# Performance work log

Measured on AMD Instinct MI355X. Metric: run time of the kernel, lower is better.

The kernel has to match this reference:

```python
import jax, jax.numpy as jnp
import numpy as np
from jax import lax

B, DIM, H, W = 4, 256, 128, 128
KS, LOC, STRIDES_CFG, HEADS = 5, [2, 3], [1, 2], 8
C2 = DIM // 2
GK = HEADS * KS  # per-pixel dynamic kernel channels

def _kernel_map(ks, kstride, kloc):
    # replicates LSAMixer.generate_kernel_map_1d
    axes, strides, start = [0], [1], 1
    for loc, s in zip(kloc, kstride):
        for num in range(0, loc - start):
            axes.append(num * s + axes[-1] + strides[-1])
            strides.append(s)
        start = loc
    patch = (axes[-1] + strides[-1]) * 2 - 1
    full_axes = [-a for a in axes[:0:-1]] + axes
    full_strides = strides[:0:-1] + strides
    return full_axes, full_strides, patch

OFFS, STRDS, PATCH = _kernel_map(KS, STRIDES_CFG, LOC)
PAD = PATCH // 2

def _pw(x, w, b):
    # 1x1 conv as GEMM
    return jnp.einsum('bchw,oc->bohw', x, w) + b[None, :, None, None]

def _dw(x, w, b, ph, pw):
    # depthwise conv, torch OIHW layout with I=1
    y = lax.conv_general_dilated(x, w, (1, 1), [(ph, ph), (pw, pw)],
                                 feature_group_count=x.shape[1],
                                 dimension_numbers=('NCHW', 'OIHW', 'NCHW'))
    return y + b[None, :, None, None]

def _fsa(x, kern, groups, axis):
    # dynamic local attention: for each tap k (offset a, stride s) gather the
    # average of x over the s-wide strided window along `axis`, weight it by
    # the per-head dynamic kernel, and accumulate.
    Bx, Cx, Hx, Wx = x.shape
    gd = Cx // groups
    K = len(OFFS)
    L = x.shape[axis]
    padcfg = [(0, 0)] * 4
    padcfg[axis] = (PAD, PAD)
    xp = jnp.pad(x, padcfg)
    taps = []
    for a, s in zip(OFFS, STRDS):
        start = a if a >= 0 else a - s + 1  # window covers s pixels away from center
        acc = lax.slice_in_dim(xp, PAD + start, PAD + start + L, axis=axis)
        for d in range(1, s):
            acc = acc + lax.slice_in_dim(xp, PAD + start + d, PAD + start + d + L, axis=axis)
        taps.append(acc / s)
    t = jnp.stack(taps, 0).reshape(K, Bx, groups, gd, Hx, Wx)
    k = kern.reshape(Bx, groups, K, Hx, Wx)
    return jnp.einsum('kbgdhw,bgkhw->bgdhw', t, k).reshape(Bx, Cx, Hx, Wx)

def setup_inputs() -> dict:
    key = jax.random.key(0)
    ks = jax.random.split(key, 12)
    sc = 0.02
    f32 = jnp.float32
    return {
        'x': jax.random.normal(ks[0], (B, DIM, H, W), f32),
        'proj_in_w': jax.random.normal(ks[1], (DIM, DIM), f32) * sc,
        'proj_in_b': jnp.zeros((DIM,), f32),
        'hk_dw_w': jax.random.normal(ks[2], (C2, 1, 1, PATCH), f32) * sc,
        'hk_dw_b': jnp.zeros((C2,), f32),
        'hk_pw_w': jax.random.normal(ks[3], (GK, C2), f32) * sc,
        'hk_pw_b': jnp.zeros((GK,), f32),
        'vk_dw_w': jax.random.normal(ks[4], (C2, 1, PATCH, 1), f32) * sc,
        'vk_dw_b': jnp.zeros((C2,), f32),
        'vk_pw_w': jax.random.normal(ks[5], (GK, C2), f32) * sc,
        'vk_pw_b': jnp.zeros((GK,), f32),
        'cb_w1': jax.random.normal(ks[6], (DIM // 4, C2), f32) * sc,
        'cb_b1': jnp.zeros((DIM // 4,), f32),
        'cb_w2': jax.random.normal(ks[7], (C2, DIM // 4), f32) * sc,
        'cb_b2': jnp.zeros((C2,), f32),
        'proj_out_w': jax.random.normal(ks[8], (DIM, DIM), f32) * sc,
        'proj_out_b': jnp.zeros((DIM,), f32),
    }

def reference(x, proj_in_w, proj_in_b, hk_dw_w, hk_dw_b, hk_pw_w, hk_pw_b,
              vk_dw_w, vk_dw_b, vk_pw_w, vk_pw_b, cb_w1, cb_b1, cb_w2, cb_b2,
              proj_out_w, proj_out_b):
    Bv, _, Hv, Wv = x.shape
    h = _pw(x, proj_in_w, proj_in_b)
    x1, x2 = h[:, :C2], h[:, C2:]
    # channel branch: pw -> relu -> pw
    x_conv = _pw(jax.nn.relu(_pw(x1, cb_w1, cb_b1)), cb_w2, cb_b2)
    # horizontal dynamic kernel + fsa
    kh = jnp.tanh(_pw(_dw(x2, hk_dw_w, hk_dw_b, 0, PAD), hk_pw_w, hk_pw_b))
    attn_h = _fsa(x2, kh, HEADS, axis=3)
    # vertical dynamic kernel + fsa
    kv = jnp.tanh(_pw(_dw(attn_h, vk_dw_w, vk_dw_b, PAD, 0), vk_pw_w, vk_pw_b))
    attn = _fsa(attn_h, kv, HEADS, axis=2)
    N = Hv * Wv
    xc = x_conv.reshape(Bv, C2, N)
    at = attn.reshape(Bv, C2, N)
    # SpatialInteraction(x_conv, attn): modulates x_conv
    s_sig = jax.nn.sigmoid(jnp.einsum('bc,bcn->bn', at.mean(-1), xc) / C2)[:, None, :]
    spatial_map = (s_sig * xc).reshape(Bv, C2, Hv, Wv)
    # ChannelInteraction(x_conv, attn): modulates attn
    c_sig = jax.nn.sigmoid(jnp.einsum('bcn,bn->bc', at, xc.mean(1)) / N)[:, :, None]
    channel_map = (c_sig * at).reshape(Bv, C2, Hv, Wv)
    out = jnp.concatenate([spatial_map, channel_map], axis=1)
    return _pw(out, proj_out_w, proj_out_b)
```

## Files before the change

### kernel.cpp

```cpp
#include <hip/hip_runtime.h>
#include <hip/hip_bf16.h>
#include <math.h>

typedef __hip_bfloat16 bf16;
typedef __attribute__((ext_vector_type(8))) short short8;
typedef __attribute__((ext_vector_type(4))) float floatx4;
#define DEV __device__ __forceinline__

constexpr int BATCH = 4;
constexpr int DIM   = 256;
constexpr int C2    = 128;
constexpr int GK    = 40;
constexpr int HH    = 128;
constexpr int WW    = 128;
constexpr int NPIX  = HH * WW;
constexpr int TPB   = 256;

DEV float toF(float v) { return v; }
DEV float toF(bf16 v)  { return __bfloat162float(v); }

DEV unsigned short f2bs(float f) {
  union { bf16 h; unsigned short u; } cv;
  cv.h = __float2bfloat16(f);
  return cv.u;
}
DEV float bs2f(unsigned short u) {
  union { float f; unsigned x; } c;
  c.x = ((unsigned)u) << 16;
  return c.f;
}

template<int N>
DEV void load_f32v(const float* __restrict__ p, float* v) {
  if constexpr (N == 8) {
    const float4 a = *(const float4*)p;
    const float4 b = *(const float4*)(p + 4);
    v[0]=a.x; v[1]=a.y; v[2]=a.z; v[3]=a.w; v[4]=b.x; v[5]=b.y; v[6]=b.z; v[7]=b.w;
  } else if constexpr (N == 4) {
    const float4 a = *(const float4*)p;
    v[0]=a.x; v[1]=a.y; v[2]=a.z; v[3]=a.w;
  } else {
    const float2 a = *(const float2*)p;
    v[0]=a.x; v[1]=a.y;
  }
}
template<int N>
DEV void load_bf16v(const bf16* __restrict__ p, float* v) {
  if constexpr (N == 8) {
    const uint4 u = *(const uint4*)p;
    v[0]=bs2f(u.x & 0xffff); v[1]=bs2f(u.x >> 16);
    v[2]=bs2f(u.y & 0xffff); v[3]=bs2f(u.y >> 16);
    v[4]=bs2f(u.z & 0xffff); v[5]=bs2f(u.z >> 16);
    v[6]=bs2f(u.w & 0xffff); v[7]=bs2f(u.w >> 16);
  } else if constexpr (N == 4) {
    const uint2 u = *(const uint2*)p;
    v[0]=bs2f(u.x & 0xffff); v[1]=bs2f(u.x >> 16);
    v[2]=bs2f(u.y & 0xffff); v[3]=bs2f(u.y >> 16);
  } else {
    const unsigned u = *(const unsigned*)p;
    v[0]=bs2f(u & 0xffff); v[1]=bs2f(u >> 16);
  }
}
DEV void load8bf(const bf16* __restrict__ p, float* v) { load_bf16v<8>(p, v); }

__global__ __launch_bounds__(TPB) void prepack_kernel(
    const float* __restrict__ w0, const float* __restrict__ w1,
    const float* __restrict__ w2, const float* __restrict__ w3,
    const float* __restrict__ w4, const float* __restrict__ w5,
    short* __restrict__ dst) {
  const int i = blockIdx.x * TPB + threadIdx.x;
  if (i >= 157696) return;
  int j = i;
  float v;
  if (j < 65536) v = w0[j];
  else if ((j -= 65536) < 8192) v = w1[j];
  else if ((j -= 8192) < 8192) v = w2[j];
  else if ((j -= 8192) < 5120) v = w3[j];
  else if ((j -= 5120) < 5120) v = w4[j];
  else { j -= 5120; v = w5[j]; }
  dst[i] = (short)f2bs(v);
}

template<int K, int O, int ACT, int GATED, int DW, typename TIN, typename TOUT>
__global__ __launch_bounds__(TPB) void pw2_kernel(
    const TIN* __restrict__ in, int in_bs,
    const short* __restrict__ wbf, const float* __restrict__ bias,
    TOUT* __restrict__ out, int out_bs,
    const bf16* __restrict__ gxc, const bf16* __restrict__ gattn,
    const float* __restrict__ gs, const float* __restrict__ gc,
    const float* __restrict__ dww, const float* __restrict__ dwb) {
  constexpr int C8   = K / 8;
  constexpr int PXT  = K / 32;
  constexpr int PG   = 64 / PXT;
  constexpr int ROWB = K * 2 + 16;
  constexpr int WO   = (O + 63) / 64;
  static_assert(DW == 0 || PXT == 4, "DW fusion assumes K=128 staging shape");
  __shared__ char smem[64 * ROWB];

  const int p0   = blockIdx.x * 64;
  const int b    = blockIdx.y;
  const int t    = threadIdx.x;
  const int lane = t & 63, wid = t >> 6;
  const int q    = lane >> 4, i16 = lane & 15;

  {
    const int c8  = t / PG;
    const int px0 = (t % PG) * PXT;
    float vals[8][PXT];
    if constexpr (DW == 1) {
      const int p = p0 + px0;
      const int row = p >> 7, w0 = p & (WW - 1);
#pragma unroll
      for (int j = 0; j < 8; ++j) {
        const int c = c8 * 8 + j;
        const float* xr = (const float*)in + ((size_t)b * C2 + c) * NPIX + row * WW;
        float xs[10];
        if (w0 > 0) { const float4 L = *(const float4*)(xr + w0 - 4); xs[0]=L.y; xs[1]=L.z; xs[2]=L.w; }
        else { xs[0]=xs[1]=xs[2]=0.f; }
        { const float4 A = *(const float4*)(xr + w0); xs[3]=A.x; xs[4]=A.y; xs[5]=A.z; xs[6]=A.w; }
        if (w0 < WW - 4) { const float4 R = *(const float4*)(xr + w0 + 4); xs[7]=R.x; xs[8]=R.y; xs[9]=R.z; }
        else { xs[7]=xs[8]=xs[9]=0.f; }
        float wv[7];
#pragma unroll
        for (int k = 0; k < 7; ++k) wv[k] = dww[c * 7 + k];
        const float bv = dwb[c];
#pragma unroll
        for (int px = 0; px < PXT; ++px) {
          float a = bv;
#pragma unroll
          for (int k = 0; k < 7; ++k) a = fmaf(wv[k], xs[px + k], a);
          vals[j][px] = a;
        }
      }
    } else if constexpr (DW == 2) {
      const int p = p0 + px0;
      const int row = p >> 7, w0 = p & (WW - 1);
#pragma unroll
      for (int j = 0; j < 8; ++j) {
        const int c = c8 * 8 + j;
        const bf16* base = (const bf16*)in + ((size_t)b * C2 + c) * NPIX + w0;
        float rr[7][PXT];
#pragma unroll
        for (int k = 0; k < 7; ++k) {
          const int hq = row - 3 + k;
          if (hq >= 0 && hq < HH) load_bf16v<PXT>(base + (size_t)hq * WW, rr[k]);
          else
#pragma unroll
            for (int px = 0; px < PXT; ++px) rr[k][px] = 0.f;
        }
        float wv[7];
#pragma unroll
        for (int k = 0; k < 7; ++k) wv[k] = dww[c * 7 + k];
        const float bv = dwb[c];
#pragma unroll
        for (int px = 0; px < PXT; ++px) {
          float a = bv;
#pragma unroll
          for (int k = 0; k < 7; ++k) a = fmaf(wv[k], rr[k][px], a);
          vals[j][px] = a;
        }
      }
    } else {
      float svals[PXT];
      if constexpr (GATED) {
        if (c8 < C8 / 2) load_f32v<PXT>(gs + (size_t)b * NPIX + p0 + px0, svals);
      }
#pragma unroll
      for (int j = 0; j < 8; ++j) {
        const int c = c8 * 8 + j;
        float tmp[PXT];
        if constexpr (GATED) {
          if (c < C2) {
            load_bf16v<PXT>(gxc + ((size_t)b * C2 + c) * NPIX + p0 + px0, tmp);
#pragma unroll
            for (int px = 0; px < PXT; ++px) vals[j][px] = tmp[px] * svals[px];
          } else {
            const float cg = gc[b * C2 + (c - C2)];
            load_bf16v<PXT>(gattn + ((size_t)b * C2 + (c - C2)) * NPIX + p0 + px0, tmp);
#pragma unroll
            for (int px = 0; px < PXT; ++px) vals[j][px] = tmp[px] * cg;
          }
        } else {
          const TIN* src = in + ((size_t)b * in_bs + c) * NPIX + p0 + px0;
          if constexpr (sizeof(TIN) == 4) load_f32v<PXT>((const float*)src, tmp);
          else                            load_bf16v<PXT>((const bf16*)src, tmp);
#pragma unroll
          for (int px = 0; px < PXT; ++px) vals[j][px] = tmp[px];
        }
      }
    }
#pragma unroll
    for (int px = 0; px < PXT; ++px) {
      const int p = px0 + px;
      short8 pk;
#pragma unroll
      for (int j = 0; j < 8; ++j) pk[j] = (short)f2bs(vals[j][px]);
      const int phys = c8 ^ ((p >> 3) & 7);
      *reinterpret_cast<short8*>(smem + (size_t)p * ROWB + phys * 16) = pk;
    }
  }
  __syncthreads();

  const int o_base = wid * WO * 16;
  if (o_base >= O) return;

  floatx4 acc[WO][4];
#pragma unroll
  for (int ot = 0; ot < WO; ++ot)
#pragma unroll
    for (int nt = 0; nt < 4; ++nt)
      acc[ot][nt] = (floatx4){0.f, 0.f, 0.f, 0.f};

  for (int kc = 0; kc < K / 32; ++kc) {
    short8 afrag[WO];
#pragma unroll
    for (int ot = 0; ot < WO; ++ot) {
      int o = o_base + ot * 16 + i16;
      if (o >= O) o = O - 1;
      afrag[ot] = *reinterpret_cast<const short8*>(wbf + (size_t)o * K + kc * 32 + q * 8);
    }
    short8 bfrag[4];
#pragma unroll
    for (int nt = 0; nt < 4; ++nt) {
      const int n = nt * 16 + i16;
      const int phys = (kc * 4 + q) ^ ((n >> 3) & 7);
      bfrag[nt] = *reinterpret_cast<const short8*>(smem + (size_t)n * ROWB + phys * 16);
    }
#pragma unroll
    for (int ot = 0; ot < WO; ++ot)
#pragma unroll
      for (int nt = 0; nt < 4; ++nt)
        acc[ot][nt] = __builtin_amdgcn_mfma_f32_16x16x32_bf16(
            afrag[ot], bfrag[nt], acc[ot][nt], 0, 0, 0);
  }

#pragma unroll
  for (int ot = 0; ot < WO; ++ot) {
#pragma unroll
    for (int reg = 0; reg < 4; ++reg) {
      const int o = o_base + ot * 16 + q * 4 + reg;
      if (o < O) {
        const float bv = bias[o];
#pragma unroll
        for (int nt = 0; nt < 4; ++nt) {
          float v = acc[ot][nt][reg] + bv;
          if (ACT == 1) v = fmaxf(v, 0.0f);
          if (ACT == 2) v = tanhf(v);
          TOUT* dst = out + ((size_t)b * out_bs + o) * NPIX + p0 + nt * 16 + i16;
          if constexpr (sizeof(TOUT) == 4) *dst = v;
          else *dst = __float2bfloat16(v);
        }
      }
    }
  }
}

__global__ __launch_bounds__(TPB) void pwfused_kernel(
    const float* __restrict__ x,
    const short* __restrict__ w_pi, const float* __restrict__ pib,
    const short* __restrict__ w_cb1, const float* __restrict__ cbb1,
    const short* __restrict__ w_cb2, const float* __restrict__ cbb2,
    float* __restrict__ x2out, bf16* __restrict__ xconv) {
  constexpr int ROWB  = 256 * 2 + 16;
  constexpr int HROWB = 128 * 2 + 16;
  constexpr int TROWB = 64 * 2 + 16;
  __shared__ char smem[64 * ROWB];
  __shared__ char hbuf[64 * HROWB];
  __shared__ char tbuf[64 * TROWB];

  const int p0   = blockIdx.x * 64;
  const int b    = blockIdx.y;
  const int t    = threadIdx.x;
  const int lane = t & 63, wid = t >> 6;
  const int q    = lane >> 4, i16 = lane & 15;

  {
    const int c8  = t / 8;
    const int px0 = (t % 8) * 8;
    float vals[8][8];
#pragma unroll
    for (int j = 0; j < 8; ++j) {
      const int c = c8 * 8 + j;
      load_f32v<8>(x + ((size_t)b * DIM + c) * NPIX + p0 + px0, vals[j]);
    }
#pragma unroll
    for (int px = 0; px < 8; ++px) {
      const int p = px0 + px;
      short8 pk;
#pragma unroll
      for (int j = 0; j < 8; ++j) pk[j] = (short)f2bs(vals[j][px]);
      const int phys = c8 ^ ((p >> 3) & 7);
      *reinterpret_cast<short8*>(smem + (size_t)p * ROWB + phys * 16) = pk;
    }
  }
  __syncthreads();

  const int o_base = wid * 64;
  {
    floatx4 acc[4][4];
#pragma unroll
    for (int ot = 0; ot < 4; ++ot)
#pragma unroll
      for (int nt = 0; nt < 4; ++nt)
        acc[ot][nt] = (floatx4){0.f, 0.f, 0.f, 0.f};

    for (int kc = 0; kc < 8; ++kc) {
      short8 afrag[4];
#pragma unroll
      for (int ot = 0; ot < 4; ++ot) {
        const int o = o_base + ot * 16 + i16;
        afrag[ot] = *reinterpret_cast<const short8*>(w_pi + (size_t)o * 256 + kc * 32 + q * 8);
      }
      short8 bfrag[4];
#pragma unroll
      for (int nt = 0; nt < 4; ++nt) {
        const int n = nt * 16 + i16;
        const int phys = (kc * 4 + q) ^ ((n >> 3) & 7);
        bfrag[nt] = *reinterpret_cast<const short8*>(smem + (size_t)n * ROWB + phys * 16);
      }
#pragma unroll
      for (int ot = 0; ot < 4; ++ot)
#pragma unroll
        for (int nt = 0; nt < 4; ++nt)
          acc[ot][nt] = __builtin_amdgcn_mfma_f32_16x16x32_bf16(
              afrag[ot], bfrag[nt], acc[ot][nt], 0, 0, 0);
    }

#pragma unroll
    for (int ot = 0; ot < 4; ++ot) {
      const int ch0 = o_base + ot * 16 + q * 4;
      if (ch0 >= C2) {
#pragma unroll
        for (int reg = 0; reg < 4; ++reg) {
          const int o = ch0 + reg;
          const float bv = pib[o];
#pragma unroll
          for (int nt = 0; nt < 4; ++nt)
            x2out[((size_t)b * C2 + (o - C2)) * NPIX + p0 + nt * 16 + i16] =
                acc[ot][nt][reg] + bv;
        }
      } else {
        float bv4[4];
#pragma unroll
        for (int reg = 0; reg < 4; ++reg) bv4[reg] = pib[ch0 + reg];
#pragma unroll
        for (int nt = 0; nt < 4; ++nt) {
          const int px = nt * 16 + i16;
          ushort4 pk;
          pk.x = f2bs(acc[ot][nt][0] + bv4[0]);
          pk.y = f2bs(acc[ot][nt][1] + bv4[1]);
          pk.z = f2bs(acc[ot][nt][2] + bv4[2]);
          pk.w = f2bs(acc[ot][nt][3] + bv4[3]);
          const int phys = (ch0 >> 3) ^ ((px >> 3) & 7);
          *reinterpret_cast<ushort4*>(hbuf + (size_t)px * HROWB + phys * 16 +
                                      (ch0 & 7) * 2) = pk;
        }
      }
    }
  }
  __syncthreads();

  {
    floatx4 acc2[4];
#pragma unroll
    for (int nt = 0; nt < 4; ++nt) acc2[nt] = (floatx4){0.f, 0.f, 0.f, 0.f};
    const int o2b = wid * 16;
    for (int kc = 0; kc < 4; ++kc) {
      const short8 afrag = *reinterpret_cast<const short8*>(
          w_cb1 + (size_t)(o2b + i16) * 128 + kc * 32 + q * 8);
      short8 bfrag[4];
#pragma unroll
      for (int nt = 0; nt < 4; ++nt) {
        const int n = nt * 16 + i16;
        const int phys = (kc * 4 + q) ^ ((n >> 3) & 7);
        bfrag[nt] = *reinterpret_cast<const short8*>(hbuf + (size_t)n * HROWB + phys * 16);
      }
#pragma unroll
      for (int nt = 0; nt < 4; ++nt)
        acc2[nt] = __builtin_amdgcn_mfma_f32_16x16x32_bf16(afrag, bfrag[nt], acc2[nt], 0, 0, 0);
    }
    const int ch0 = o2b + q * 4;
    float bv4[4];
#pragma unroll
    for (int reg = 0; reg < 4; ++reg) bv4[reg] = cbb1[ch0 + reg];
#pragma unroll
    for (int nt = 0; nt < 4; ++nt) {
      const int px = nt * 16 + i16;
      ushort4 pk;
      pk.x = f2bs(fmaxf(acc2[nt][0] + bv4[0], 0.f));
      pk.y = f2bs(fmaxf(acc2[nt][1] + bv4[1], 0.f));
      pk.z = f2bs(fmaxf(acc2[nt][2] + bv4[2], 0.f));
      pk.w = f2bs(fmaxf(acc2[nt][3] + bv4[3], 0.f));
      const int phys = (ch0 >> 3) ^ ((px >> 3) & 7);
      *reinterpret_cast<ushort4*>(tbuf + (size_t)px * TROWB + phys * 16 +
                                  (ch0 & 7) * 2) = pk;
    }
  }
  __syncthreads();

  {
    floatx4 acc3[2][4];
#pragma unroll
    for (int ot = 0; ot < 2; ++ot)
#pragma unroll
      for (int nt = 0; nt < 4; ++nt) acc3[ot][nt] = (floatx4){0.f, 0.f, 0.f, 0.f};
    const int o3b = wid * 32;
    for (int kc = 0; kc < 2; ++kc) {
      short8 afrag[2];
#pragma unroll
      for (int ot = 0; ot < 2; ++ot)
        afrag[ot] = *reinterpret_cast<const short8*>(
            w_cb2 + (size_t)(o3b + ot * 16 + i16) * 64 + kc * 32 + q * 8);
      short8 bfrag[4];
#pragma unroll
      for (int nt = 0; nt < 4; ++nt) {
        const int n = nt * 16 + i16;
        const int phys = (kc * 4 + q) ^ ((n >> 3) & 7);
        bfrag[nt] = *reinterpret_cast<const short8*>(tbuf + (size_t)n * TROWB + phys * 16);
      }
#pragma unroll
      for (int ot = 0; ot < 2; ++ot)
#pragma unroll
        for (int nt = 0; nt < 4; ++nt)
          acc3[ot][nt] = __builtin_amdgcn_mfma_f32_16x16x32_bf16(
              afrag[ot], bfrag[nt], acc3[ot][nt], 0, 0, 0);
    }
#pragma unroll
    for (int ot = 0; ot < 2; ++ot) {
#pragma unroll
      for (int reg = 0; reg < 4; ++reg) {
        const int o = o3b + ot * 16 + q * 4 + reg;
        const float bv = cbb2[o];
#pragma unroll
        for (int nt = 0; nt < 4; ++nt)
          xconv[((size_t)b * C2 + o) * NPIX + p0 + nt * 16 + i16] =
              __float2bfloat16(acc3[ot][nt][reg] + bv);
      }
    }
  }
}

DEV float block_reduce_sum(float v) {
#pragma unroll
  for (int off = 32; off > 0; off >>= 1) v += __shfl_down(v, off, 64);
  __shared__ float ls[TPB / 64];
  const int lane = threadIdx.x & 63;
  const int wid  = threadIdx.x >> 6;
  if (lane == 0) ls[wid] = v;
  __syncthreads();
  float s = 0.0f;
  if (threadIdx.x == 0) {
#pragma unroll
    for (int i = 0; i < TPB / 64; ++i) s += ls[i];
  }
  return s;
}

__global__ __launch_bounds__(TPB) void fsah2_kernel(
    const float* __restrict__ x, int x_bs,
    const bf16* __restrict__ kern, bf16* __restrict__ out) {
  const int g  = blockIdx.x * TPB + threadIdx.x;
  const int w8 = g & 15;
  const int hp = (g >> 4) & (HH - 1);
  const int c  = (g >> 11) & (C2 - 1);
  const int b  = g >> 18;
  const float* xr = x + ((size_t)b * x_bs + c) * NPIX + hp * WW;
  const int px0 = w8 * 8;
  float xs[14];
  if (w8 > 0) { const float4 L = *(const float4*)(xr + px0 - 4); xs[0]=L.y; xs[1]=L.z; xs[2]=L.w; }
  else { xs[0]=xs[1]=xs[2]=0.f; }
  { const float4 a = *(const float4*)(xr + px0);
    const float4 bq = *(const float4*)(xr + px0 + 4);
    xs[3]=a.x; xs[4]=a.y; xs[5]=a.z; xs[6]=a.w;
    xs[7]=bq.x; xs[8]=bq.y; xs[9]=bq.z; xs[10]=bq.w; }
  if (w8 < 15) { const float4 R = *(const float4*)(xr + px0 + 8); xs[11]=R.x; xs[12]=R.y; xs[13]=R.z; }
  else { xs[11]=xs[12]=xs[13]=0.f; }
  float k[5][8];
  const bf16* kr = kern + ((size_t)b * GK + (c >> 4) * 5) * NPIX + hp * WW + px0;
#pragma unroll
  for (int tp = 0; tp < 5; ++tp) load8bf(kr + (size_t)tp * NPIX, k[tp]);
  short8 o;
#pragma unroll
  for (int i = 0; i < 8; ++i) {
    float a = 0.5f * (xs[i] + xs[i + 1]) * k[0][i];
    a = fmaf(xs[i + 2], k[1][i], a);
    a = fmaf(xs[i + 3], k[2][i], a);
    a = fmaf(xs[i + 4], k[3][i], a);
    a = fmaf(0.5f * (xs[i + 5] + xs[i + 6]), k[4][i], a);
    o[i] = (short)f2bs(a);
  }
  *reinterpret_cast<short8*>(out + ((size_t)(b * C2 + c)) * NPIX + hp * WW + px0) = o;
}

__global__ __launch_bounds__(TPB) void fsav2_kernel(
    const bf16* __restrict__ x,
    const bf16* __restrict__ kern, bf16* __restrict__ out,
    float* __restrict__ at_mean) {
  const int g  = blockIdx.x * TPB + threadIdx.x;
  const int w8 = g & 15;
  const int hp = (g >> 4) & (HH - 1);
  const int c  = (g >> 11) & (C2 - 1);
  const int b  = g >> 18;
  const int px0 = w8 * 8;
  const bf16* base = x + ((size_t)(b * C2 + c)) * NPIX + px0;
  float r[7][8];
#pragma unroll
  for (int j = 0; j < 7; ++j) {
    const int hq = hp - 3 + j;
    if (hq >= 0 && hq < HH) load8bf(base + (size_t)hq * WW, r[j]);
    else
#pragma unroll
      for (int i = 0; i < 8; ++i) r[j][i] = 0.f;
  }
  float k[5][8];
  const bf16* kr = kern + ((size_t)b * GK + (c >> 4) * 5) * NPIX + hp * WW + px0;
#pragma unroll
  for (int tp = 0; tp < 5; ++tp) load8bf(kr + (size_t)tp * NPIX, k[tp]);
  short8 o;
  float ps = 0.0f;
#pragma unroll
  for (int i = 0; i < 8; ++i) {
    float a = 0.5f * (r[0][i] + r[1][i]) * k[0][i];
    a = fmaf(r[2][i], k[1][i], a);
    a = fmaf(r[3][i], k[2][i], a);
    a = fmaf(r[4][i], k[3][i], a);
    a = fmaf(0.5f * (r[5][i] + r[6][i]), k[4][i], a);
    o[i] = (short)f2bs(a);
    ps += bs2f((unsigned short)o[i]);
  }
  *reinterpret_cast<short8*>(out + ((size_t)(b * C2 + c)) * NPIX + hp * WW + px0) = o;
  const float s = block_reduce_sum(ps);
  if (threadIdx.x == 0) atomicAdd(&at_mean[b * C2 + c], s);
}

__global__ __launch_bounds__(TPB) void xs_kernel(const bf16* __restrict__ xc,
                                                 const float* __restrict__ at_mean,
                                                 float* __restrict__ xc_mean,
                                                 float* __restrict__ s_sig) {
  __shared__ float am[C2];
  const int b = blockIdx.y;
  if (threadIdx.x < C2) am[threadIdx.x] = at_mean[b * C2 + threadIdx.x] * (1.0f / NPIX);
  __syncthreads();
  const int p = blockIdx.x * TPB + threadIdx.x;
  const bf16* r = xc + (size_t)b * C2 * NPIX + p;
  float s = 0.0f, m = 0.0f;
#pragma unroll 4
  for (int c = 0; c < C2; ++c) {
    const float v = toF(r[(size_t)c * NPIX]);
    m += v;
    s = fmaf(am[c], v, s);
  }
  xc_mean[(size_t)b * NPIX + p] = m * (1.0f / C2);
  s_sig[(size_t)b * NPIX + p]   = 1.0f / (1.0f + expf(-s * (1.0f / C2)));
}

__global__ __launch_bounds__(TPB) void csig_kernel(const bf16* __restrict__ attn,
                                                   const float* __restrict__ xc_mean,
                                                   float* __restrict__ out) {
  const int bc = blockIdx.x;
  const int b  = bc / C2;
  const bf16* r = attn + (size_t)bc * NPIX;
  const float* m = xc_mean + (size_t)b * NPIX;
  float s = 0.0f;
  for (int i = threadIdx.x * 8; i < NPIX; i += TPB * 8) {
    float v[8], mm[8];
    load8bf(r + i, v);
    load_f32v<8>(m + i, mm);
#pragma unroll
    for (int j = 0; j < 8; ++j) s = fmaf(v[j], mm[j], s);
  }
  s = block_reduce_sum(s);
  if (threadIdx.x == 0) out[bc] = 1.0f / (1.0f + expf(-s * (1.0f / NPIX)));
}

extern "C" void kernel_launch(void* const* d_in, const int* in_sizes, int n_in,
                              void* d_out, int out_size, void* d_ws, size_t ws_size,
                              hipStream_t stream) {
  const float* x    = (const float*)d_in[0];
  const float* piw  = (const float*)d_in[1];
  const float* pib  = (const float*)d_in[2];
  const float* hkdw = (const float*)d_in[3];
  const float* hkdb = (const float*)d_in[4];
  const float* hkpw = (const float*)d_in[5];
  const float* hkpb = (const float*)d_in[6];
  const float* vkdw = (const float*)d_in[7];
  const float* vkdb = (const float*)d_in[8];
  const float* vkpw = (const float*)d_in[9];
  const float* vkpb = (const float*)d_in[10];
  const float* cbw1 = (const float*)d_in[11];
  const float* cbb1 = (const float*)d_in[12];
  const float* cbw2 = (const float*)d_in[13];
  const float* cbb2 = (const float*)d_in[14];
  const float* pow_ = (const float*)d_in[15];
  const float* pob  = (const float*)d_in[16];
  float* out = (float*)d_out;

  char* ws = (char*)d_ws;
  size_t off = 0;
  auto alloc = [&](size_t bytes) -> char* {
    char* p = ws + off;
    off += (bytes + 255) & ~(size_t)255;
    return p;
  };
  short* wpk    = (short*)alloc(157696 * 2);
  float* x2buf  = (float*)alloc((size_t)BATCH * C2  * NPIX * 4);
  bf16*  x_conv = (bf16*) alloc((size_t)BATCH * C2  * NPIX * 2);
  bf16*  kbuf   = (bf16*) alloc((size_t)BATCH * GK  * NPIX * 2);
  bf16*  attn_h = (bf16*) alloc((size_t)BATCH * C2  * NPIX * 2);
  bf16*  attn   = (bf16*) alloc((size_t)BATCH * C2  * NPIX * 2);
  float* at_mean = (float*)alloc((size_t)BATCH * C2 * 4);
  float* xc_mean = (float*)alloc((size_t)BATCH * NPIX * 4);
  float* s_sig   = (float*)alloc((size_t)BATCH * NPIX * 4);
  float* c_sig   = (float*)alloc((size_t)BATCH * C2 * 4);

  const short* w_pi  = wpk;
  const short* w_cb1 = wpk + 65536;
  const short* w_cb2 = wpk + 73728;
  const short* w_hk  = wpk + 81920;
  const short* w_vk  = wpk + 87040;
  const short* w_po  = wpk + 92160;

  const dim3 blk(TPB);
  const dim3 gemm_grid(NPIX / 64, BATCH);
  const int PT  = NPIX / TPB;
  const int EL8 = BATCH * C2 * HH * 16 / TPB;

  prepack_kernel<<<dim3((157696 + TPB - 1) / TPB), blk, 0, stream>>>(
      piw, cbw1, cbw2, hkpw, vkpw, pow_, wpk);
  hipMemsetAsync(at_mean, 0, (size_t)BATCH * C2 * 4, stream);
  pwfused_kernel<<<gemm_grid, blk, 0, stream>>>(
      x, w_pi, pib, w_cb1, cbb1, w_cb2, cbb2, x2buf, x_conv);
  pw2_kernel<128, 40, 2, 0, 1, float, bf16><<<gemm_grid, blk, 0, stream>>>(
      x2buf, C2, w_hk, hkpb, kbuf, GK, nullptr, nullptr, nullptr, nullptr, hkdw, hkdb);
  fsah2_kernel<<<dim3(EL8), blk, 0, stream>>>(x2buf, C2, kbuf, attn_h);
  pw2_kernel<128, 40, 2, 0, 2, bf16, bf16><<<gemm_grid, blk, 0, stream>>>(
      attn_h, C2, w_vk, vkpb, kbuf, GK, nullptr, nullptr, nullptr, nullptr, vkdw, vkdb);
  fsav2_kernel<<<dim3(EL8), blk, 0, stream>>>(attn_h, kbuf, attn, at_mean);
  xs_kernel<<<dim3(PT, BATCH), blk, 0, stream>>>(x_conv, at_mean, xc_mean, s_sig);
  csig_kernel<<<dim3(BATCH * C2), blk, 0, stream>>>(attn, xc_mean, c_sig);
  pw2_kernel<256, 256, 0, 1, 0, bf16, float><<<gemm_grid, blk, 0, stream>>>(
      x_conv, 0, w_po, pob, out, DIM, x_conv, attn, s_sig, c_sig, nullptr, nullptr);
}
```

Baseline: 346.9 us.

## Fuse dynamic-kernel generation with FSA application per image row

Two new kernels, one per direction, each compute the depthwise conv, the pointwise MFMA GEMM with tanh, and the strided attention for one image row inside a single block. The per-pixel dynamic kernel stays in shared memory, so the global kbuf write and read-back and two kernel launches go away. In exchange each row block reloads its input from global memory twice. The grid shrinks to 512 blocks with larger shared memory per block, which may lower occupancy.

After: 378.2 us. 9.0% more time.

```diff
diff --git a/kernel.cpp b/kernel.cpp
--- a/kernel.cpp
+++ b/kernel.cpp
@@ -81,20 +81,18 @@
   dst[i] = (short)f2bs(v);
 }
 
-template<int K, int O, int ACT, int GATED, int DW, typename TIN, typename TOUT>
+template<int K, int O, int ACT, int GATED, typename TIN, typename TOUT>
 __global__ __launch_bounds__(TPB) void pw2_kernel(
     const TIN* __restrict__ in, int in_bs,
     const short* __restrict__ wbf, const float* __restrict__ bias,
     TOUT* __restrict__ out, int out_bs,
     const bf16* __restrict__ gxc, const bf16* __restrict__ gattn,
-    const float* __restrict__ gs, const float* __restrict__ gc,
-    const float* __restrict__ dww, const float* __restrict__ dwb) {
+    const float* __restrict__ gs, const float* __restrict__ gc) {
   constexpr int C8   = K / 8;
   constexpr int PXT  = K / 32;
   constexpr int PG   = 64 / PXT;
   constexpr int ROWB = K * 2 + 16;
   constexpr int WO   = (O + 63) / 64;
-  static_assert(DW == 0 || PXT == 4, "DW fusion assumes K=128 staging shape");
   __shared__ char smem[64 * ROWB];
 
   const int p0   = blockIdx.x * 64;
@@ -107,86 +105,31 @@
     const int c8  = t / PG;
     const int px0 = (t % PG) * PXT;
     float vals[8][PXT];
-    if constexpr (DW == 1) {
-      const int p = p0 + px0;
-      const int row = p >> 7, w0 = p & (WW - 1);
-#pragma unroll
-      for (int j = 0; j < 8; ++j) {
-        const int c = c8 * 8 + j;
-        const float* xr = (const float*)in + ((size_t)b * C2 + c) * NPIX + row * WW;
-        float xs[10];
-        if (w0 > 0) { const float4 L = *(const float4*)(xr + w0 - 4); xs[0]=L.y; xs[1]=L.z; xs[2]=L.w; }
-        else { xs[0]=xs[1]=xs[2]=0.f; }
-        { const float4 A = *(const float4*)(xr + w0); xs[3]=A.x; xs[4]=A.y; xs[5]=A.z; xs[6]=A.w; }
-        if (w0 < WW - 4) { const float4 R = *(const float4*)(xr + w0 + 4); xs[7]=R.x; xs[8]=R.y; xs[9]=R.z; }
-        else { xs[7]=xs[8]=xs[9]=0.f; }
-        float wv[7];
-#pragma unroll
-        for (int k = 0; k < 7; ++k) wv[k] = dww[c * 7 + k];
-        const float bv = dwb[c];
-#pragma unroll
-        for (int px = 0; px < PXT; ++px) {
-          float a = bv;
-#pragma unroll
-          for (int k = 0; k < 7; ++k) a = fmaf(wv[k], xs[px + k], a);
-          vals[j][px] = a;
+    float svals[PXT];
+    if constexpr (GATED) {
+      if (c8 < C8 / 2) load_f32v<PXT>(gs + (size_t)b * NPIX + p0 + px0, svals);
+    }
+#pragma unroll
+    for (int j = 0; j < 8; ++j) {
+      const int c = c8 * 8 + j;
+      float tmp[PXT];
+      if constexpr (GATED) {
+        if (c < C2) {
+          load_bf16v<PXT>(gxc + ((size_t)b * C2 + c) * NPIX + p0 + px0, tmp);
+#pragma unroll
+          for (int px = 0; px < PXT; ++px) vals[j][px] = tmp[px] * svals[px];
+        } else {
+          const float cg = gc[b * C2 + (c - C2)];
+          load_bf16v<PXT>(gattn + ((size_t)b * C2 + (c - C2)) * NPIX + p0 + px0, tmp);
+#pragma unroll
+          for (int px = 0; px < PXT; ++px) vals[j][px] = tmp[px] * cg;
         }
-      }
-    } else if constexpr (DW == 2) {
-      const int p = p0 + px0;
-      const int row = p >> 7, w0 = p & (WW - 1);
-#pragma unroll
-      for (int j = 0; j < 8; ++j) {
-        const int c = c8 * 8 + j;
-        const bf16* base = (const bf16*)in + ((size_t)b * C2 + c) * NPIX + w0;
-        float rr[7][PXT];
-#pragma unroll
-        for (int k = 0; k < 7; ++k) {
-          const int hq = row - 3 + k;
-          if (hq >= 0 && hq < HH) load_bf16v<PXT>(base + (size_t)hq * WW, rr[k]);
-          else
-#pragma unroll
-            for (int px = 0; px < PXT; ++px) rr[k][px] = 0.f;
-        }
-        float wv[7];
-#pragma unroll
-        for (int k = 0; k < 7; ++k) wv[k] = dww[c * 7 + k];
-        const float bv = dwb[c];
-#pragma unroll
-        for (int px = 0; px < PXT; ++px) {
-          float a = bv;
-#pragma unroll
-          for (int k = 0; k < 7; ++k) a = fmaf(wv[k], rr[k][px], a);
-          vals[j][px] = a;
-        }
-      }
-    } else {
-      float svals[PXT];
-      if constexpr (GATED) {
-        if (c8 < C8 / 2) load_f32v<PXT>(gs + (size_t)b * NPIX + p0 + px0, svals);
-      }
-#pragma unroll
-      for (int j = 0; j < 8; ++j) {
-        const int c = c8 * 8 + j;
-        float tmp[PXT];
-        if constexpr (GATED) {
-          if (c < C2) {
-            load_bf16v<PXT>(gxc + ((size_t)b * C2 + c) * NPIX + p0 + px0, tmp);
-#pragma unroll
-            for (int px = 0; px < PXT; ++px) vals[j][px] = tmp[px] * svals[px];
-          } else {
-            const float cg = gc[b * C2 + (c - C2)];
-            load_bf16v<PXT>(gattn + ((size_t)b * C2 + (c - C2)) * NPIX + p0 + px0, tmp);
-#pragma unroll
-            for (int px = 0; px < PXT; ++px) vals[j][px] = tmp[px] * cg;
-          }
-        } else {
-          const TIN* src = in + ((size_t)b * in_bs + c) * NPIX + p0 + px0;
-          if constexpr (sizeof(TIN) == 4) load_f32v<PXT>((const float*)src, tmp);
-          else                            load_bf16v<PXT>((const bf16*)src, tmp);
-#pragma unroll
-          for (int px = 0; px < PXT; ++px) vals[j][px] = tmp[px];
-        }
+      } else {
+        const TIN* src = in + ((size_t)b * in_bs + c) * NPIX + p0 + px0;
+        if constexpr (sizeof(TIN) == 4) load_f32v<PXT>((const float*)src, tmp);
+        else                            load_bf16v<PXT>((const bf16*)src, tmp);
+#pragma unroll
+        for (int px = 0; px < PXT; ++px) vals[j][px] = tmp[px];
       }
     }
 #pragma unroll
@@ -440,6 +383,306 @@
   }
 }
 
+__global__ __launch_bounds__(TPB) void hkfused_kernel(
+    const float* __restrict__ x2,
+    const float* __restrict__ dw7, const float* __restrict__ dwb,
+    const short* __restrict__ wpw, const float* __restrict__ pwb,
+    bf16* __restrict__ outp) {
+  constexpr int ROWB  = 128 * 2 + 16;
+  constexpr int KROWB = 128 * 2 + 16;
+  __shared__ char dws[128 * ROWB];
+  __shared__ char khs[GK * KROWB];
+
+  const int row  = blockIdx.x;
+  const int b    = blockIdx.y;
+  const int t    = threadIdx.x;
+  const int lane = t & 63, wid = t >> 6;
+  const int q    = lane >> 4, i16 = lane & 15;
+  const int c8   = t >> 4;
+  const int px0  = (t & 15) * 8;
+
+  {
+    float vals[8][8];
+#pragma unroll
+    for (int j = 0; j < 8; ++j) {
+      const int c = c8 * 8 + j;
+      const float* xr = x2 + ((size_t)b * C2 + c) * NPIX + row * WW;
+      float xs[14];
+      if (px0 > 0) { const float4 L = *(const float4*)(xr + px0 - 4); xs[0]=L.y; xs[1]=L.z; xs[2]=L.w; }
+      else { xs[0]=xs[1]=xs[2]=0.f; }
+      { const float4 a = *(const float4*)(xr + px0);
+        const float4 bq = *(const float4*)(xr + px0 + 4);
+        xs[3]=a.x; xs[4]=a.y; xs[5]=a.z; xs[6]=a.w;
+        xs[7]=bq.x; xs[8]=bq.y; xs[9]=bq.z; xs[10]=bq.w; }
+      if (px0 < 120) { const float4 R = *(const float4*)(xr + px0 + 8); xs[11]=R.x; xs[12]=R.y; xs[13]=R.z; }
+      else { xs[11]=xs[12]=xs[13]=0.f; }
+      float wv[7];
+#pragma unroll
+      for (int k = 0; k < 7; ++k) wv[k] = dw7[c * 7 + k];
+      const float bv = dwb[c];
+#pragma unroll
+      for (int i = 0; i < 8; ++i) {
+        float a = bv;
+#pragma unroll
+        for (int k = 0; k < 7; ++k) a = fmaf(wv[k], xs[i + k], a);
+        vals[j][i] = a;
+      }
+    }
+#pragma unroll
+    for (int i = 0; i < 8; ++i) {
+      const int p = px0 + i;
+      short8 pk;
+#pragma unroll
+      for (int j = 0; j < 8; ++j) pk[j] = (short)f2bs(vals[j][i]);
+      const int phys = c8 ^ ((p >> 3) & 7);
+      *reinterpret_cast<short8*>(dws + (size_t)p * ROWB + phys * 16) = pk;
+    }
+  }
+  __syncthreads();
+
+  {
+    const int n0 = wid * 32;
+    floatx4 acc[3][2];
+#pragma unroll
+    for (int ot = 0; ot < 3; ++ot)
+#pragma unroll
+      for (int nt = 0; nt < 2; ++nt) acc[ot][nt] = (floatx4){0.f, 0.f, 0.f, 0.f};
+    for (int kc = 0; kc < 4; ++kc) {
+      short8 afrag[3];
+#pragma unroll
+      for (int ot = 0; ot < 3; ++ot) {
+        int o = ot * 16 + i16;
+        if (o >= GK) o = GK - 1;
+        afrag[ot] = *reinterpret_cast<const short8*>(wpw + (size_t)o * 128 + kc * 32 + q * 8);
+      }
+      short8 bfrag[2];
+#pragma unroll
+      for (int nt = 0; nt < 2; ++nt) {
+        const int n = n0 + nt * 16 + i16;
+        const int phys = (kc * 4 + q) ^ ((n >> 3) & 7);
+        bfrag[nt] = *reinterpret_cast<const short8*>(dws + (size_t)n * ROWB + phys * 16);
+      }
+#pragma unroll
+      for (int ot = 0; ot < 3; ++ot)
+#pragma unroll
+        for (int nt = 0; nt < 2; ++nt)
+          acc[ot][nt] = __builtin_amdgcn_mfma_f32_16x16x32_bf16(
+              afrag[ot], bfrag[nt], acc[ot][nt], 0, 0, 0);
+    }
+#pragma unroll
+    for (int ot = 0; ot < 3; ++ot) {
+#pragma unroll
+      for (int reg = 0; reg < 4; ++reg) {
+        const int o = ot * 16 + q * 4 + reg;
+        if (o < GK) {
+          const float bv = pwb[o];
+#pragma unroll
+          for (int nt = 0; nt < 2; ++nt) {
+            const int px = n0 + nt * 16 + i16;
+            *reinterpret_cast<unsigned short*>(khs + (size_t)o * KROWB + px * 2) =
+                f2bs(tanhf(acc[ot][nt][reg] + bv));
+          }
+        }
+      }
+    }
+  }
+  __syncthreads();
+
+  {
+    const int g = c8 >> 1;
+    float k5[5][8];
+#pragma unroll
+    for (int tp = 0; tp < 5; ++tp) {
+      const short8 kv = *reinterpret_cast<const short8*>(
+          khs + (size_t)(g * 5 + tp) * KROWB + px0 * 2);
+#pragma unroll
+      for (int i = 0; i < 8; ++i) k5[tp][i] = bs2f((unsigned short)kv[i]);
+    }
+#pragma unroll
+    for (int j = 0; j < 8; ++j) {
+      const int c = c8 * 8 + j;
+      const float* xr = x2 + ((size_t)b * C2 + c) * NPIX + row * WW;
+      float xs[14];
+      if (px0 > 0) { const float4 L = *(const float4*)(xr + px0 - 4); xs[0]=L.y; xs[1]=L.z; xs[2]=L.w; }
+      else { xs[0]=xs[1]=xs[2]=0.f; }
+      { const float4 a = *(const float4*)(xr + px0);
+        const float4 bq = *(const float4*)(xr + px0 + 4);
+        xs[3]=a.x; xs[4]=a.y; xs[5]=a.z; xs[6]=a.w;
+        xs[7]=bq.x; xs[8]=bq.y; xs[9]=bq.z; xs[10]=bq.w; }
+      if (px0 < 120) { const float4 R = *(const float4*)(xr + px0 + 8); xs[11]=R.x; xs[12]=R.y; xs[13]=R.z; }
+      else { xs[11]=xs[12]=xs[13]=0.f; }
+      short8 o8;
+#pragma unroll
+      for (int i = 0; i < 8; ++i) {
+        float a = 0.5f * (xs[i] + xs[i + 1]) * k5[0][i];
+        a = fmaf(xs[i + 2], k5[1][i], a);
+        a = fmaf(xs[i + 3], k5[2][i], a);
+        a = fmaf(xs[i + 4], k5[3][i], a);
+        a = fmaf(0.5f * (xs[i + 5] + xs[i + 6]), k5[4][i], a);
+        o8[i] = (short)f2bs(a);
+      }
+      *reinterpret_cast<short8*>(outp + ((size_t)(b * C2 + c)) * NPIX + row * WW + px0) = o8;
+    }
+  }
+}
+
+__global__ __launch_bounds__(TPB) void vkfused_kernel(
+    const bf16* __restrict__ ah,
+    const float* __restrict__ dw7, const float* __restrict__ dwb,
+    const short* __restrict__ wpw, const float* __restrict__ pwb,
+    bf16* __restrict__ outp, float* __restrict__ at_mean) {
+  constexpr int ROWB  = 128 * 2 + 16;
+  constexpr int KROWB = 128 * 2 + 16;
+  __shared__ char dws[128 * ROWB];
+  __shared__ char khs[GK * KROWB];
+
+  const int row  = blockIdx.x;
+  const int b    = blockIdx.y;
+  const int t    = threadIdx.x;
+  const int lane = t & 63, wid = t >> 6;
+  const int q    = lane >> 4, i16 = lane & 15;
+  const int c8   = t >> 4;
+  const int px0  = (t & 15) * 8;
+
+  {
+    float vals[8][8];
+#pragma unroll
+    for (int j = 0; j < 8; ++j) {
+      const int c = c8 * 8 + j;
+      const bf16* base = ah + ((size_t)b * C2 + c) * NPIX + px0;
+      float r[7][8];
+#pragma unroll
+      for (int k = 0; k < 7; ++k) {
+        const int hq = row - 3 + k;
+        if (hq >= 0 && hq < HH) load8bf(base + (size_t)hq * WW, r[k]);
+        else
+#pragma unroll
+          for (int i = 0; i < 8; ++i) r[k][i] = 0.f;
+      }
+      float wv[7];
+#pragma unroll
+      for (int k = 0; k < 7; ++k) wv[k] = dw7[c * 7 + k];
+      const float bv = dwb[c];
+#pragma unroll
+      for (int i = 0; i < 8; ++i) {
+        float a = bv;
+#pragma unroll
+        for (int k = 0; k < 7; ++k) a = fmaf(wv[k], r[k][i], a);
+        vals[j][i] = a;
+      }
+    }
+#pragma unroll
+    for (int i = 0; i < 8; ++i) {
+      const int p = px0 + i;
+      short8 pk;
+#pragma unroll
+      for (int j = 0; j < 8; ++j) pk[j] = (short)f2bs(vals[j][i]);
+      const int phys = c8 ^ ((p >> 3) & 7);
+      *reinterpret_cast<short8*>(dws + (size_t)p * ROWB + phys * 16) = pk;
+    }
+  }
+  __syncthreads();
+
+  {
+    const int n0 = wid * 32;
+    floatx4 acc[3][2];
+#pragma unroll
+    for (int ot = 0; ot < 3; ++ot)
+#pragma unroll
+      for (int nt = 0; nt < 2; ++nt) acc[ot][nt] = (floatx4){0.f, 0.f, 0.f, 0.f};
+    for (int kc = 0; kc < 4; ++kc) {
+      short8 afrag[3];
+#pragma unroll
+      for (int ot = 0; ot < 3; ++ot) {
+        int o = ot * 16 + i16;
+        if (o >= GK) o = GK - 1;
+        afrag[ot] = *reinterpret_cast<const short8*>(wpw + (size_t)o * 128 + kc * 32 + q * 8);
+      }
+      short8 bfrag[2];
+#pragma unroll
+      for (int nt = 0; nt < 2; ++nt) {
+        const int n = n0 + nt * 16 + i16;
+        const int phys = (kc * 4 + q) ^ ((n >> 3) & 7);
+        bfrag[nt] = *reinterpret_cast<const short8*>(dws + (size_t)n * ROWB + phys * 16);
+      }
+#pragma unroll
+      for (int ot = 0; ot < 3; ++ot)
+#pragma unroll
+        for (int nt = 0; nt < 2; ++nt)
+          acc[ot][nt] = __builtin_amdgcn_mfma_f32_16x16x32_bf16(
+              afrag[ot], bfrag[nt], acc[ot][nt], 0, 0, 0);
+    }
+#pragma unroll
+    for (int ot = 0; ot < 3; ++ot) {
+#pragma unroll
+      for (int reg = 0; reg < 4; ++reg) {
+        const int o = ot * 16 + q * 4 + reg;
+        if (o < GK) {
+          const float bv = pwb[o];
+#pragma unroll
+          for (int nt = 0; nt < 2; ++nt) {
+            const int px = n0 + nt * 16 + i16;
+            *reinterpret_cast<unsigned short*>(khs + (size_t)o * KROWB + px * 2) =
+                f2bs(tanhf(acc[ot][nt][reg] + bv));
+          }
+        }
+      }
+    }
+  }
+  __syncthreads();
+
+  {
+    const int g = c8 >> 1;
+    float k5[5][8];
+#pragma unroll
+    for (int tp = 0; tp < 5; ++tp) {
+      const short8 kv = *reinterpret_cast<const short8*>(
+          khs + (size_t)(g * 5 + tp) * KROWB + px0 * 2);
+#pragma unroll
+      for (int i = 0; i < 8; ++i) k5[tp][i] = bs2f((unsigned short)kv[i]);
+    }
+    float psum[8];
+#pragma unroll
+    for (int j = 0; j < 8; ++j) {
+      const int c = c8 * 8 + j;
+      const bf16* base = ah + ((size_t)b * C2 + c) * NPIX + px0;
+      float r[7][8];
+#pragma unroll
+      for (int k = 0; k < 7; ++k) {
+        const int hq = row - 3 + k;
+        if (hq >= 0 && hq < HH) load8bf(base + (size_t)hq * WW, r[k]);
+        else
+#pragma unroll
+          for (int i = 0; i < 8; ++i) r[k][i] = 0.f;
+      }
+      short8 o8;
+      float ps = 0.0f;
+#pragma unroll
+      for (int i = 0; i < 8; ++i) {
+        float a = 0.5f * (r[0][i] + r[1][i]) * k5[0][i];
+        a = fmaf(r[2][i], k5[1][i], a);
+        a = fmaf(r[3][i], k5[2][i], a);
+        a = fmaf(r[4][i], k5[3][i], a);
+        a = fmaf(0.5f * (r[5][i] + r[6][i]), k5[4][i], a);
+        o8[i] = (short)f2bs(a);
+        ps += bs2f((unsigned short)o8[i]);
+      }
+      *reinterpret_cast<short8*>(outp + ((size_t)(b * C2 + c)) * NPIX + row * WW + px0) = o8;
+      psum[j] = ps;
+    }
+#pragma unroll
+    for (int j = 0; j < 8; ++j) {
+#pragma unroll
+      for (int off = 8; off > 0; off >>= 1) psum[j] += __shfl_down(psum[j], off, 16);
+    }
+    if ((t & 15) == 0) {
+#pragma unroll
+      for (int j = 0; j < 8; ++j)
+        atomicAdd(&at_mean[b * C2 + c8 * 8 + j], psum[j]);
+    }
+  }
+}
+
 DEV float block_reduce_sum(float v) {
 #pragma unroll
   for (int off = 32; off > 0; off >>= 1) v += __shfl_down(v, off, 64);
@@ -454,83 +697,6 @@
     for (int i = 0; i < TPB / 64; ++i) s += ls[i];
   }
   return s;
-}
-
-__global__ __launch_bounds__(TPB) void fsah2_kernel(
-    const float* __restrict__ x, int x_bs,
-    const bf16* __restrict__ kern, bf16* __restrict__ out) {
-  const int g  = blockIdx.x * TPB + threadIdx.x;
-  const int w8 = g & 15;
-  const int hp = (g >> 4) & (HH - 1);
-  const int c  = (g >> 11) & (C2 - 1);
-  const int b  = g >> 18;
-  const float* xr = x + ((size_t)b * x_bs + c) * NPIX + hp * WW;
-  const int px0 = w8 * 8;
-  float xs[14];
-  if (w8 > 0) { const float4 L = *(const float4*)(xr + px0 - 4); xs[0]=L.y; xs[1]=L.z; xs[2]=L.w; }
-  else { xs[0]=xs[1]=xs[2]=0.f; }
-  { const float4 a = *(const float4*)(xr + px0);
-    const float4 bq = *(const float4*)(xr + px0 + 4);
-    xs[3]=a.x; xs[4]=a.y; xs[5]=a.z; xs[6]=a.w;
-    xs[7]=bq.x; xs[8]=bq.y; xs[9]=bq.z; xs[10]=bq.w; }
-  if (w8 < 15) { const float4 R = *(const float4*)(xr + px0 + 8); xs[11]=R.x; xs[12]=R.y; xs[13]=R.z; }
-  else { xs[11]=xs[12]=xs[13]=0.f; }
-  float k[5][8];
-  const bf16* kr = kern + ((size_t)b * GK + (c >> 4) * 5) * NPIX + hp * WW + px0;
-#pragma unroll
-  for (int tp = 0; tp < 5; ++tp) load8bf(kr + (size_t)tp * NPIX, k[tp]);
-  short8 o;
-#pragma unroll
-  for (int i = 0; i < 8; ++i) {
-    float a = 0.5f * (xs[i] + xs[i + 1]) * k[0][i];
-    a = fmaf(xs[i + 2], k[1][i], a);
-    a = fmaf(xs[i + 3], k[2][i], a);
-    a = fmaf(xs[i + 4], k[3][i], a);
-    a = fmaf(0.5f * (xs[i + 5] + xs[i + 6]), k[4][i], a);
-    o[i] = (short)f2bs(a);
-  }
-  *reinterpret_cast<short8*>(out + ((size_t)(b * C2 + c)) * NPIX + hp * WW + px0) = o;
-}
-
-__global__ __launch_bounds__(TPB) void fsav2_kernel(
-    const bf16* __restrict__ x,
-    const bf16* __restrict__ kern, bf16* __restrict__ out,
-    float* __restrict__ at_mean) {
-  const int g  = blockIdx.x * TPB + threadIdx.x;
-  const int w8 = g & 15;
-  const int hp = (g >> 4) & (HH - 1);
-  const int c  = (g >> 11) & (C2 - 1);
-  const int b  = g >> 18;
-  const int px0 = w8 * 8;
-  const bf16* base = x + ((size_t)(b * C2 + c)) * NPIX + px0;
-  float r[7][8];
-#pragma unroll
-  for (int j = 0; j < 7; ++j) {
-    const int hq = hp - 3 + j;
-    if (hq >= 0 && hq < HH) load8bf(base + (size_t)hq * WW, r[j]);
-    else
-#pragma unroll
-      for (int i = 0; i < 8; ++i) r[j][i] = 0.f;
-  }
-  float k[5][8];
-  const bf16* kr = kern + ((size_t)b * GK + (c >> 4) * 5) * NPIX + hp * WW + px0;
-#pragma unroll
-  for (int tp = 0; tp < 5; ++tp) load8bf(kr + (size_t)tp * NPIX, k[tp]);
-  short8 o;
-  float ps = 0.0f;
-#pragma unroll
-  for (int i = 0; i < 8; ++i) {
-    float a = 0.5f * (r[0][i] + r[1][i]) * k[0][i];
-    a = fmaf(r[2][i], k[1][i], a);
-    a = fmaf(r[3][i], k[2][i], a);
-    a = fmaf(r[4][i], k[3][i], a);
-    a = fmaf(0.5f * (r[5][i] + r[6][i]), k[4][i], a);
-    o[i] = (short)f2bs(a);
-    ps += bs2f((unsigned short)o[i]);
-  }
-  *reinterpret_cast<short8*>(out + ((size_t)(b * C2 + c)) * NPIX + hp * WW + px0) = o;
-  const float s = block_reduce_sum(ps);
-  if (threadIdx.x == 0) atomicAdd(&at_mean[b * C2 + c], s);
 }
 
 __global__ __launch_bounds__(TPB) void xs_kernel(const bf16* __restrict__ xc,
@@ -605,7 +771,6 @@
   short* wpk    = (short*)alloc(157696 * 2);
   float* x2buf  = (float*)alloc((size_t)BATCH * C2  * NPIX * 4);
   bf16*  x_conv = (bf16*) alloc((size_t)BATCH * C2  * NPIX * 2);
-  bf16*  kbuf   = (bf16*) alloc((size_t)BATCH * GK  * NPIX * 2);
   bf16*  attn_h = (bf16*) alloc((size_t)BATCH * C2  * NPIX * 2);
   bf16*  attn   = (bf16*) alloc((size_t)BATCH * C2  * NPIX * 2);
   float* at_mean = (float*)alloc((size_t)BATCH * C2 * 4);
@@ -622,22 +787,20 @@
 
   const dim3 blk(TPB);
   const dim3 gemm_grid(NPIX / 64, BATCH);
+  const dim3 row_grid(HH, BATCH);
   const int PT  = NPIX / TPB;
-  const int EL8 = BATCH * C2 * HH * 16 / TPB;
 
   prepack_kernel<<<dim3((157696 + TPB - 1) / TPB), blk, 0, stream>>>(
       piw, cbw1, cbw2, hkpw, vkpw, pow_, wpk);
   hipMemsetAsync(at_mean, 0, (size_t)BATCH * C2 * 4, stream);
   pwfused_kernel<<<gemm_grid, blk, 0, stream>>>(
       x, w_pi, pib, w_cb1, cbb1, w_cb2, cbb2, x2buf, x_conv);
-  pw2_kernel<128, 40, 2, 0, 1, float, bf16><<<gemm_grid, blk, 0, stream>>>(
-      x2buf, C2, w_hk, hkpb, kbuf, GK, nullptr, nullptr, nullptr, nullptr, hkdw, hkdb);
-  fsah2_kernel<<<dim3(EL8), blk, 0, stream>>>(x2buf, C2, kbuf, attn_h);
-  pw2_kernel<128, 40, 2, 0, 2, bf16, bf16><<<gemm_grid, blk, 0, stream>>>(
-      attn_h, C2, w_vk, vkpb, kbuf, GK, nullptr, nullptr, nullptr, nullptr, vkdw, vkdb);
-  fsav2_kernel<<<dim3(EL8), blk, 0, stream>>>(attn_h, kbuf, attn, at_mean);
+  hkfused_kernel<<<row_grid, blk, 0, stream>>>(
+      x2buf, hkdw, hkdb, w_hk, hkpb, attn_h);
+  vkfused_kernel<<<row_grid, blk, 0, stream>>>(
+      attn_h, vkdw, vkdb, w_vk, vkpb, attn, at_mean);
   xs_kernel<<<dim3(PT, BATCH), blk, 0, stream>>>(x_conv, at_mean, xc_mean, s_sig);
   csig_kernel<<<dim3(BATCH * C2), blk, 0, stream>>>(attn, xc_mean, c_sig);
-  pw2_kernel<256, 256, 0, 1, 0, bf16, float><<<gemm_grid, blk, 0, stream>>>(
-      x_conv, 0, w_po, pob, out, DIM, x_conv, attn, s_sig, c_sig, nullptr, nullptr);
-}
+  pw2_kernel<256, 256, 0, 1, bf16, float><<<gemm_grid, blk, 0, stream>>>(
+      x_conv, 0, w_po, pob, out, DIM, x_conv, attn, s_sig, c_sig);
+}
```
